# Kernel optimization log

Measured on AMD Instinct MI355X. Metric: run time of the kernel, lower is better.

## Reference

```python
import jax, jax.numpy as jnp
import numpy as np

B, N, D, H = 64, 196, 768, 3072
QMAX = 127.0  # 8-bit symmetric: clamp to [-128, 127]


def ste_round(x):
    # straight-through-estimator round (QAT)
    return x + jax.lax.stop_gradient(jnp.round(x) - x)


def q_linear_diag(x, w, b, a_sf):
    """Quantized diagonal linear (ResMLP Affine / LayerScale as QuantLinear)."""
    w_sf = jnp.max(jnp.abs(w)) / QMAX            # per-tensor weight scale
    w_int = ste_round(w / w_sf)                  # int8 weights (|.|<=127)
    out_int = (x / a_sf) * w_int
    if b is not None:
        out_int = out_int + ste_round(b / (a_sf * w_sf))  # 32-bit bias
    return out_int * (a_sf * w_sf), w_sf


def q_linear_dense(x, w, b, a_sf):
    """Quantized dense linear: int8 GEMM + int32 bias, dequant with a_sf*w_sf."""
    w_sf = jnp.max(jnp.abs(w)) / QMAX
    w_int = jnp.clip(ste_round(w / w_sf), -QMAX - 1, QMAX)
    out_int = jnp.einsum('...i,oi->...o', x / a_sf, w_int) + ste_round(b / (a_sf * w_sf))
    return out_int * (a_sf * w_sf), w_sf


def q_act(x, pre_sf, new_sf, identity=None, id_sf=None):
    """HAWQ-style QuantAct: fixed-point requantization to scale new_sf (8-bit)."""
    if identity is None:
        z_int = ste_round(x / pre_sf)
        out_int = ste_round(z_int * (pre_sf / new_sf))
    else:
        # main branch (x - identity) requantized with pre_sf, identity with id_sf
        z_int = ste_round((x - identity) / pre_sf)
        out_int = ste_round(z_int * (pre_sf / new_sf)) \
                + ste_round(ste_round(identity / id_sf) * (id_sf / new_sf))
    out_int = jnp.clip(out_int, -QMAX - 1, QMAX)
    return out_int * new_sf, new_sf


def _forward(x, norm1_w, norm1_b, attn_w, attn_b, gamma1_w,
             norm2_w, norm2_b, fc1_w, fc1_b, fc2_w, fc2_b, gamma2_w, act_sfs):
    a_sf = act_sfs[0]
    # --- token-mixing half ---
    identity, id_sf = x, a_sf
    x, w_sf = q_linear_diag(x, norm1_w, norm1_b, a_sf)         # norm1 (affine)
    x = jnp.swapaxes(x, 1, 2)                                  # [B, D, N]
    x, a_sf = q_act(x, a_sf * w_sf, act_sfs[1])                # quant_act1
    x, w_sf = q_linear_dense(x, attn_w, attn_b, a_sf)          # attn (cross-patch)
    x = jnp.swapaxes(x, 1, 2)                                  # [B, N, D]
    x, a_sf = q_act(x, a_sf * w_sf, act_sfs[2])                # quant_act2
    x, w_sf = q_linear_diag(x, gamma1_w, None, a_sf)           # gamma_1 (layerscale)
    x = x + identity
    x, a_sf = q_act(x, a_sf * w_sf, act_sfs[3], identity, id_sf)  # quant_act_int32_1
    # --- MLP half ---
    identity, id_sf = x, a_sf
    x, w_sf = q_linear_diag(x, norm2_w, norm2_b, a_sf)         # norm2
    x, a_sf = q_act(x, a_sf * w_sf, act_sfs[4])                # quant_act3
    x, w_sf = q_linear_dense(x, fc1_w, fc1_b, a_sf)            # mlp.fc1
    x = jax.nn.relu(x)
    x, a_sf = q_act(x, a_sf * w_sf, act_sfs[5])                # mlp.quant_act1
    x, w_sf = q_linear_dense(x, fc2_w, fc2_b, a_sf)            # mlp.fc2
    x, a_sf = q_act(x, a_sf * w_sf, act_sfs[6])                # mlp.quant_act2
    x, w_sf = q_linear_diag(x, gamma2_w, None, a_sf)           # gamma_2
    x = x + identity
    x, a_sf = q_act(x, a_sf * w_sf, act_sfs[7], identity, id_sf)  # quant_act_int32_2
    return x, a_sf


def setup_inputs() -> dict:
    key = jax.random.key(0)
    ks = jax.random.split(key, 16)
    act_sfs = jax.random.uniform(ks[14], (8,), jnp.float32, 0.02, 0.06)
    x = jax.random.normal(ks[0], (B, N, D), jnp.float32)
    # input is already quantized at scale act_sfs[0]
    x = jnp.clip(jnp.round(x / act_sfs[0]), -128, 127) * act_sfs[0]
    s = 0.05
    return {
        'x': x,
        'norm1_w': 1.0 + s * jax.random.normal(ks[1], (D,), jnp.float32),
        'norm1_b': s * jax.random.normal(ks[2], (D,), jnp.float32),
        'attn_w': jax.random.normal(ks[3], (N, N), jnp.float32) / np.sqrt(N),
        'attn_b': s * jax.random.normal(ks[4], (N,), jnp.float32),
        'gamma1_w': 0.1 + s * jax.random.normal(ks[5], (D,), jnp.float32),
        'norm2_w': 1.0 + s * jax.random.normal(ks[6], (D,), jnp.float32),
        'norm2_b': s * jax.random.normal(ks[7], (D,), jnp.float32),
        'fc1_w': jax.random.normal(ks[8], (H, D), jnp.float32) / np.sqrt(D),
        'fc1_b': s * jax.random.normal(ks[9], (H,), jnp.float32),
        'fc2_w': jax.random.normal(ks[10], (D, H), jnp.float32) / np.sqrt(H),
        'fc2_b': s * jax.random.normal(ks[11], (D,), jnp.float32),
        'gamma2_w': 0.1 + s * jax.random.normal(ks[12], (D,), jnp.float32),
        'act_sfs': act_sfs,
    }


def reference(x, norm1_w, norm1_b, attn_w, attn_b, gamma1_w,
              norm2_w, norm2_b, fc1_w, fc1_b, fc2_w, fc2_b, gamma2_w, act_sfs):
    return _forward(x, norm1_w, norm1_b, attn_w, attn_b, gamma1_w,
                    norm2_w, norm2_b, fc1_w, fc1_b, fc2_w, fc2_b, gamma2_w, act_sfs)
```

## Files before the change

kernel.cpp:

```cpp
#include <hip/hip_runtime.h>

#define B_ 64
#define N_ 196
#define D_ 768
#define H_ 3072
#define M_ (B_*N_)
#define NP 256

typedef int int4v  __attribute__((ext_vector_type(4)));
typedef int int16v __attribute__((ext_vector_type(16)));
typedef signed char i8;

#define WS_MAX 0
#define WS_W1F 16
#define WS_B1F (16+768)
#define WS_G1F (16+768*2)
#define WS_W2F (16+768*3)
#define WS_B2F (16+768*4)
#define WS_G2F (16+768*5)
#define WS_BA  (16+768*6)
#define WS_BF1 (WS_BA+256)
#define WS_BF2 (WS_BF1+3072)
#define OFF_WA   40960ull
#define OFF_FC1  (OFF_WA+65536ull)
#define OFF_FC2  (OFF_FC1+2359296ull)
#define OFF_X2   (OFF_FC2+2359296ull)
#define OFF_Q3   (OFF_X2+9633792ull)
#define OFF_Q4   (OFF_Q3+9633792ull)
#define OFF_Q1T  OFF_Q4
#define OFF_X8   (OFF_Q4+12582912ull)

__device__ __forceinline__ float clamp8(float v){ return fminf(fmaxf(v,-128.f),127.f); }

__device__ __forceinline__ void async16(const void* g, void* l){
    __builtin_amdgcn_global_load_lds((const __attribute__((address_space(1))) void*)g,
                                     (__attribute__((address_space(3))) void*)l, 16, 0, 0);
}

__global__ void k_init(char* ws, const float* __restrict__ act, float* out_tail){
    int id = blockIdx.x*256 + threadIdx.x;
    if (blockIdx.x == 0){
        float* f = (float*)ws;
        if (threadIdx.x < 8) f[WS_MAX+threadIdx.x] = 0.f;
        if (threadIdx.x == 8) *out_tail = act[7];
    }
    if (id < 4096){ int4v z = {0,0,0,0}; ((int4v*)(ws+OFF_WA))[id] = z; }
}

__global__ void k_maxabs(const float* __restrict__ p0, const float* __restrict__ p1,
                         const float* __restrict__ p2, const float* __restrict__ p3,
                         const float* __restrict__ p4, const float* __restrict__ p5,
                         const float* __restrict__ p6, float* wsmax){
    const float* ps[7] = {p0,p1,p2,p3,p4,p5,p6};
    const int    n4s[7] = {192, 9604, 192, 192, 589824, 589824, 192};
    int tid = blockIdx.y;
    const float4* p = (const float4*)ps[tid]; int n4 = n4s[tid];
    float m = 0.f;
    for (int i = blockIdx.x*blockDim.x + threadIdx.x; i < n4; i += gridDim.x*blockDim.x){
        float4 v = p[i];
        m = fmaxf(m, fmaxf(fmaxf(fabsf(v.x),fabsf(v.y)), fmaxf(fabsf(v.z),fabsf(v.w))));
    }
    #pragma unroll
    for (int off = 32; off; off >>= 1) m = fmaxf(m, __shfl_down(m, off, 64));
    __shared__ float red[4];
    int lane = threadIdx.x & 63, wv = threadIdx.x >> 6;
    if (lane == 0) red[wv] = m;
    __syncthreads();
    if (threadIdx.x == 0){
        float mm = red[0];
        for (int w = 1; w < (int)blockDim.x/64; w++) mm = fmaxf(mm, red[w]);
        atomicMax((unsigned*)&wsmax[tid], __float_as_uint(mm));
    }
}

__device__ __forceinline__ size_t cm_off(int o, int k, int KC){
    return (((size_t)(o>>7)*KC + (k>>6))<<13) + (((k>>4)&3)<<11) + ((o&127)<<4) + (k&15);
}

__global__ void k_qweights(const float* __restrict__ n1w, const float* __restrict__ n1b,
                           const float* __restrict__ aw,  const float* __restrict__ ab,
                           const float* __restrict__ g1w, const float* __restrict__ n2w,
                           const float* __restrict__ n2b, const float* __restrict__ f1w,
                           const float* __restrict__ f1b, const float* __restrict__ f2w,
                           const float* __restrict__ f2b, const float* __restrict__ g2w,
                           const float* __restrict__ act, char* ws){
    float* fws = (float*)ws;
    int*   iws = (int*)ws;
    const float* mx = fws + WS_MAX;
    long i = (long)blockIdx.x*blockDim.x + threadIdx.x;
    const long F4 = 589824;
    if (i < F4){ float sf = mx[4]/127.0f;
        float4 v = ((const float4*)f1w)[i];
        int o = (int)(i/192), kb = (int)(i%192)*4;
        unsigned b0 = (unsigned)(unsigned char)(i8)(int)fminf(fmaxf(rintf(v.x/sf),-128.f),127.f);
        unsigned b1 = (unsigned)(unsigned char)(i8)(int)fminf(fmaxf(rintf(v.y/sf),-128.f),127.f);
        unsigned b2 = (unsigned)(unsigned char)(i8)(int)fminf(fmaxf(rintf(v.z/sf),-128.f),127.f);
        unsigned b3 = (unsigned)(unsigned char)(i8)(int)fminf(fmaxf(rintf(v.w/sf),-128.f),127.f);
        *(unsigned*)(ws + OFF_FC1 + cm_off(o, kb, 12)) = b0 | (b1<<8) | (b2<<16) | (b3<<24);
        return; }
    i -= F4;
    if (i < F4){ float sf = mx[5]/127.0f;
        float4 v = ((const float4*)f2w)[i];
        int o = (int)(i/768), kb = (int)(i%768)*4;
        unsigned b0 = (unsigned)(unsigned char)(i8)(int)fminf(fmaxf(rintf(v.x/sf),-128.f),127.f);
        unsigned b1 = (unsigned)(unsigned char)(i8)(int)fminf(fmaxf(rintf(v.y/sf),-128.f),127.f);
        unsigned b2 = (unsigned)(unsigned char)(i8)(int)fminf(fmaxf(rintf(v.z/sf),-128.f),127.f);
        unsigned b3 = (unsigned)(unsigned char)(i8)(int)fminf(fmaxf(rintf(v.w/sf),-128.f),127.f);
        *(unsigned*)(ws + OFF_FC2 + cm_off(o, kb, 48)) = b0 | (b1<<8) | (b2<<16) | (b3<<24);
        return; }
    i -= F4;
    if (i < 38416){ float sf = mx[1]/127.0f;
        int o = (int)(i/196), k = (int)(i%196);
        ((i8*)(ws+OFF_WA))[cm_off(o, k, 4)] =
            (i8)(int)fminf(fmaxf(rintf(aw[i]/sf),-128.f),127.f); return; }
    i -= 38416;
    if (i < 768){ float sf = mx[0]/127.0f; fws[WS_W1F+i] = rintf(n1w[i]/sf); return; }
    i -= 768;
    if (i < 768){ float sf = mx[0]/127.0f; fws[WS_B1F+i] = rintf(n1b[i]/(act[0]*sf)); return; }
    i -= 768;
    if (i < 768){ float sf = mx[2]/127.0f; fws[WS_G1F+i] = rintf(g1w[i]/sf); return; }
    i -= 768;
    if (i < 768){ float sf = mx[3]/127.0f; fws[WS_W2F+i] = rintf(n2w[i]/sf); return; }
    i -= 768;
    if (i < 768){ float sf = mx[3]/127.0f; fws[WS_B2F+i] = rintf(n2b[i]/(act[3]*sf)); return; }
    i -= 768;
    if (i < 768){ float sf = mx[6]/127.0f; fws[WS_G2F+i] = rintf(g2w[i]/sf); return; }
    i -= 768;
    if (i < 196){ float sf = mx[1]/127.0f; iws[WS_BA+i] = (int)rintf(ab[i]/(act[1]*sf)); return; }
    i -= 196;
    if (i < 3072){ float sf = mx[4]/127.0f; iws[WS_BF1+i] = (int)rintf(f1b[i]/(act[4]*sf)); return; }
    i -= 3072;
    if (i < 768){ float sf = mx[5]/127.0f; iws[WS_BF2+i] = (int)rintf(f2b[i]/(act[5]*sf)); return; }
}

__global__ __launch_bounds__(256) void k_stage1(const float* __restrict__ x,
                                                const char* __restrict__ wsc,
                                                char* __restrict__ ws,
                                                const float* __restrict__ act){
    __shared__ i8 T[64][68];
    const float* fws = (const float*)wsc;
    int b = blockIdx.z, n0 = blockIdx.y*64, d0 = blockIdx.x*64;
    int t = threadIdx.x;
    float a0 = act[0];
    float w1sf = fws[WS_MAX+0]/127.0f;
    float r1 = (a0*w1sf)/act[1];
    int dl = (t & 15) * 4;
    int d  = d0 + dl;
    float4 wv = *(const float4*)(fws + WS_W1F + d);
    float4 bv = *(const float4*)(fws + WS_B1F + d);
    i8* x8 = (i8*)(ws + OFF_X8);
    #pragma unroll
    for (int pass = 0; pass < 4; pass++){
        int nl = (t >> 4) + pass*16;
        int n  = n0 + nl;
        i8 q[4] = {0,0,0,0};
        if (n < 196){
            float4 xv = *(const float4*)(x + ((size_t)b*196 + n)*768 + d);
            float i0 = rintf(xv.x/a0), i1 = rintf(xv.y/a0);
            float i2 = rintf(xv.z/a0), i3 = rintf(xv.w/a0);
            *(char4*)(x8 + ((size_t)b*196 + n)*768 + d) =
                make_char4((i8)(int)i0,(i8)(int)i1,(i8)(int)i2,(i8)(int)i3);
            float o0 = rintf(i0*wv.x + bv.x);
            float o1 = rintf(i1*wv.y + bv.y);
            float o2 = rintf(i2*wv.z + bv.z);
            float o3 = rintf(i3*wv.w + bv.w);
            q[0] = (i8)(int)clamp8(rintf(o0*r1));
            q[1] = (i8)(int)clamp8(rintf(o1*r1));
            q[2] = (i8)(int)clamp8(rintf(o2*r1));
            q[3] = (i8)(int)clamp8(rintf(o3*r1));
        }
        T[dl+0][nl] = q[0]; T[dl+1][nl] = q[1];
        T[dl+2][nl] = q[2]; T[dl+3][nl] = q[3];
    }
    __syncthreads();
    i8* q1T = (i8*)(ws + OFF_Q1T) + (size_t)b*196608;
    #pragma unroll
    for (int e = 0; e < 4; e++){
        int id = t + e*256;
        int row = id >> 4, c = (id & 15) * 4;
        int dd = d0 + row;
        int v = *(const int*)&T[row][c];
        size_t dst = (((size_t)(dd>>7)*4 + blockIdx.y)<<13) + ((size_t)(c>>4)<<11)
                     + ((dd&127)<<4) + (c&15);
        *(int*)(q1T + dst) = v;
    }
}

__device__ __forceinline__ void gemm_cm_256(const i8* __restrict__ gA, const i8* __restrict__ gB,
                                            int iters, int4v acc[4][4], i8* As, i8* Bs, int t){
    int lane = t & 63;
    int wm = (t>>6)&1, wn = t>>7;
    int lo = t*16;
    async16(gA + lo,        As + lo);
    async16(gA + 4096 + lo, As + 4096 + lo);
    async16(gB + lo,        Bs + lo);
    async16(gB + 4096 + lo, Bs + 4096 + lo);
    int arow = (lane>>4)*2048 + (wm*64 + (lane&15))*16;
    int brow = (lane>>4)*2048 + (wn*64 + (lane&15))*16;
    for (int i = 0; i < iters; i++){
        __syncthreads();
        if (i+1 < iters){
            int nb = ((i+1)&1) << 13;
            size_t kb = (size_t)(i+1) << 13;
            async16(gA + kb + lo,        As + nb + lo);
            async16(gA + kb + 4096 + lo, As + nb + 4096 + lo);
            async16(gB + kb + lo,        Bs + nb + lo);
            async16(gB + kb + 4096 + lo, Bs + nb + 4096 + lo);
        }
        int cb = (i&1) << 13;
        int4v a[4], bb[4];
        #pragma unroll
        for (int mt = 0; mt < 4; mt++)
            a[mt] = *(const int4v*)(As + cb + arow + mt*256);
        #pragma unroll
        for (int nt = 0; nt < 4; nt++)
            bb[nt] = *(const int4v*)(Bs + cb + brow + nt*256);
        #pragma unroll
        for (int mt = 0; mt < 4; mt++)
            #pragma unroll
            for (int nt = 0; nt < 4; nt++)
                acc[mt][nt] = __builtin_amdgcn_mfma_i32_16x16x64_i8(a[mt], bb[nt], acc[mt][nt], 0,0,0);
    }
}

__device__ __forceinline__ void gemm32_cm_pipe(const i8* __restrict__ gA, const i8* __restrict__ gB,
                                               int iters, int16v acc[2][2], i8* lds, int t){
    int lane = t & 63;
    int wm = (t>>6)&1, wn = t>>7;
    int lo = t*16;
    auto stage = [&](int s, int buf){
        size_t kb = (size_t)s << 13;
        i8* L = lds + buf*16384;
        async16(gA + kb + lo,        L + lo);
        async16(gA + kb + 4096 + lo, L + 4096 + lo);
        async16(gB + kb + lo,        L + 8192 + lo);
        async16(gB + kb + 4096 + lo, L + 12288 + lo);
    };
    stage(0, 0);
    if (iters > 1) stage(1, 1);
    int arow = (lane>>5)*2048 + (wm*64 + (lane&31))*16;
    int brow = 8192 + (lane>>5)*2048 + (wn*64 + (lane&31))*16;
    int buf = 0;
    for (int i = 0; i < iters; i++){
        if (i+1 < iters) asm volatile("s_waitcnt vmcnt(4)" ::: "memory");
        else             asm volatile("s_waitcnt vmcnt(0)" ::: "memory");
        __builtin_amdgcn_s_barrier();
        __builtin_amdgcn_sched_barrier(0);
        if (i+2 < iters){
            int b2 = buf + 2; if (b2 >= 3) b2 -= 3;
            stage(i+2, b2);
        }
        const i8* L = lds + buf*16384;
        int4v a[2][2], bb[2][2];
        #pragma unroll
        for (int kk = 0; kk < 2; kk++){
            #pragma unroll
            for (int mt = 0; mt < 2; mt++){
                a[kk][mt]  = *(const int4v*)(L + kk*4096 + arow + mt*512);
                bb[kk][mt] = *(const int4v*)(L + kk*4096 + brow + mt*512);
            }
        }
        #pragma unroll
        for (int mt = 0; mt < 2; mt++)
            #pragma unroll
            for (int nt = 0; nt < 2; nt++)
                #pragma unroll
                for (int kk = 0; kk < 2; kk++)
                    acc[mt][nt] = __builtin_amdgcn_mfma_i32_32x32x32_i8(a[kk][mt], bb[kk][nt], acc[mt][nt], 0,0,0);
        buf++; if (buf == 3) buf = 0;
    }
}

__global__ __launch_bounds__(256) void k_attn(const char* __restrict__ ws,
                                              const float* __restrict__ act){
    __shared__ char smem[32768];
    const float* fws = (const float*)ws;
    const int*   iws = (const int*)ws;
    int b = blockIdx.z;
    int m0 = blockIdx.x*128, n0 = blockIdx.y*128;
    const i8* gA = (const i8*)(ws + OFF_WA)  + ((size_t)(m0>>7))*32768;
    const i8* gB = (const i8*)(ws + OFF_Q1T) + (size_t)b*196608 + ((size_t)(n0>>7))*32768;
    const i8* x8 = (const i8*)(ws + OFF_X8);
    i8* x2  = (i8*)(ws + OFF_X2);
    i8* q3  = (i8*)(ws + OFF_Q3);
    int t = threadIdx.x, lane = t & 63;
    int wm = (t>>6)&1, wn = t>>7;
    int4v acc[4][4]; int4v zz = {0,0,0,0};
    #pragma unroll
    for (int mt=0;mt<4;mt++) for (int nt=0;nt<4;nt++) acc[mt][nt] = zz;
    gemm_cm_256(gA, gB, 4, acc, (i8*)smem, (i8*)smem+16384, t);

    float a1=act[1], a2=act[2], a3=act[3], a4=act[4];
    float wasf = fws[WS_MAX+1]/127.0f; float r2  = (a1*wasf)/a2;
    float g1sf = fws[WS_MAX+2]/127.0f; float r3a = (a2*g1sf)/a3; float r3b = act[0]/a3;
    float w2sf = fws[WS_MAX+3]/127.0f; float r4  = (a3*w2sf)/a4;
    float g1v[4], w2v[4], b2v[4];
    #pragma unroll
    for (int nt=0;nt<4;nt++){
        int d = n0 + wn*64 + nt*16 + (lane&15);
        g1v[nt] = fws[WS_G1F + d]; w2v[nt] = fws[WS_W2F + d]; b2v[nt] = fws[WS_B2F + d];
    }
    __syncthreads();
    i8* Xs = (i8*)smem;
    i8* Qs = (i8*)smem + 16384;
    #pragma unroll
    for (int mt=0;mt<4;mt++){
        #pragma unroll
        for (int r=0;r<4;r++){
            int ml = wm*64 + mt*16 + (lane>>4)*4 + r;
            int o  = m0 + ml;
            int ba = iws[WS_BA + o];
            #pragma unroll
            for (int nt=0;nt<4;nt++){
                int nl = wn*64 + nt*16 + (lane&15);
                int d  = n0 + nl;
                float s2 = (float)(acc[mt][nt][r] + ba);
                float q2 = clamp8(rintf(s2*r2));
                float o3v = q2*g1v[nt];
                float idi = (o < 196) ? (float)x8[((size_t)b*196 + o)*768 + d] : 0.f;
                float tt = rintf(o3v*r3a) + rintf(idi*r3b);
                tt = clamp8(tt);
                float o4 = tt*w2v[nt] + b2v[nt];
                float qr = clamp8(rintf(o4*r4));
                Xs[ml*128 + nl] = (i8)(int)tt;
                Qs[ml*128 + nl] = (i8)(int)qr;
            }
        }
    }
    __syncthreads();
    #pragma unroll
    for (int e=0;e<4;e++){
        int id = t + e*256;
        int row = id>>3, c = id&7;
        int o = m0 + row;
        if (o < 196){
            int rg = b*196 + o;
            size_t g = (size_t)rg*768 + n0 + c*16;
            *(int4v*)(x2 + g) = *(const int4v*)(Xs + row*128 + c*16);
            size_t dst = (((size_t)(rg>>7)*12 + (n0>>6) + (c>>2))<<13)
                         + ((size_t)(c&3)<<11) + ((rg&127)<<4);
            *(int4v*)(q3 + dst) = *(const int4v*)(Qs + row*128 + c*16);
        }
    }
}

__global__ __launch_bounds__(256,3) void k_fc1(const char* __restrict__ ws, const float* __restrict__ act){
    __shared__ char smem[49152];
    const float* fws = (const float*)ws;
    const int*   iws = (const int*)ws;
    int n0 = blockIdx.y*128;
    const i8* gA = (const i8*)(ws+OFF_Q3)  + ((size_t)blockIdx.x)*12*8192;
    const i8* gB = (const i8*)(ws+OFF_FC1) + ((size_t)blockIdx.y)*12*8192;
    const int* bias = iws + WS_BF1;
    i8* q4 = (i8*)(ws+OFF_Q4);
    int t = threadIdx.x, lane = t & 63;
    int wm = (t>>6)&1, wn = t>>7;
    int16v acc[2][2];
    int16v zz = {0,0,0,0,0,0,0,0,0,0,0,0,0,0,0,0};
    #pragma unroll
    for (int mt=0;mt<2;mt++) for (int nt=0;nt<2;nt++) acc[mt][nt] = zz;
    gemm32_cm_pipe(gA, gB, 12, acc, (i8*)smem, t);
    float wsf = fws[WS_MAX+4]/127.0f;
    float r5 = (act[4]*wsf)/act[5];
    int bcol[2];
    #pragma unroll
    for (int nt=0;nt<2;nt++) bcol[nt] = bias[n0 + wn*64 + nt*32 + (lane&31)];
    i8* Cs = (i8*)smem;
    #pragma unroll
    for (int mt=0;mt<2;mt++){
        #pragma unroll
        for (int nt=0;nt<2;nt++){
            int nl = wn*64 + nt*32 + (lane&31);
            #pragma unroll
            for (int r=0;r<16;r++){
                int s = acc[mt][nt][r] + bcol[nt];
                if (s < 0) s = 0;
                float q = clamp8(rintf((float)s * r5));
                int ml = wm*64 + mt*32 + 4*(lane>>5) + (r&3) + 8*(r>>2);
                Cs[ml*128 + nl] = (i8)(int)q;
            }
        }
    }
    __syncthreads();
    #pragma unroll
    for (int e=0;e<4;e++){
        int id = t + e*256;
        int row = id>>3, c = id&7;
        size_t dst = (((size_t)blockIdx.x*48 + (n0>>6) + (c>>2))<<13)
                     + ((size_t)(c&3)<<11) + ((size_t)row<<4);
        *(int4v*)(q4 + dst) = *(const int4v*)(Cs + row*128 + c*16);
    }
}

__global__ __launch_bounds__(256,3) void k_fc2(const char* __restrict__ ws, const float* __restrict__ act,
                                               float* __restrict__ out){
    __shared__ char smem[49152];
    const float* fws = (const float*)ws;
    const int*   iws = (const int*)ws;
    int m0 = blockIdx.x*128, n0 = blockIdx.y*128;
    const i8* gA = (const i8*)(ws+OFF_Q4)  + ((size_t)blockIdx.x)*48*8192;
    const i8* gB = (const i8*)(ws+OFF_FC2) + ((size_t)blockIdx.y)*48*8192;
    const int* bias = iws + WS_BF2;
    const float* g2f = fws + WS_G2F;
    const i8* x2 = (const i8*)(ws+OFF_X2);
    int t = threadIdx.x, lane = t & 63;
    int wm = (t>>6)&1, wn = t>>7;
    int16v acc[2][2];
    int16v zz = {0,0,0,0,0,0,0,0,0,0,0,0,0,0,0,0};
    #pragma unroll
    for (int mt=0;mt<2;mt++) for (int nt=0;nt<2;nt++) acc[mt][nt] = zz;
    gemm32_cm_pipe(gA, gB, 48, acc, (i8*)smem, t);
    float a3=act[3], a5=act[5], a6=act[6], a7=act[7];
    float wsf  = fws[WS_MAX+5]/127.0f; float r6  = (a5*wsf)/a6;
    float g2sf = fws[WS_MAX+6]/127.0f; float r7a = (a6*g2sf)/a7; float r7b = a3/a7;
    int bcol[2]; float g2v[2];
    #pragma unroll
    for (int nt=0;nt<2;nt++){
        int nc = n0 + wn*64 + nt*32 + (lane&31);
        bcol[nt] = bias[nc]; g2v[nt] = g2f[nc];
    }
    #pragma unroll
    for (int mt=0;mt<2;mt++){
        #pragma unroll
        for (int nt=0;nt<2;nt++){
            int nc = n0 + wn*64 + nt*32 + (lane&31);
            #pragma unroll
            for (int r=0;r<16;r++){
                int ml = wm*64 + mt*32 + 4*(lane>>5) + (r&3) + 8*(r>>2);
                size_t gi = (size_t)(m0+ml)*768 + nc;
                int s = acc[mt][nt][r] + bcol[nt];
                float q6 = clamp8(rintf((float)s*r6));
                float o7 = q6*g2v[nt];
                float idi = (float)x2[gi];
                float tt = rintf(o7*r7a) + rintf(idi*r7b);
                tt = clamp8(tt);
                out[gi] = tt*a7;
            }
        }
    }
}

extern "C" void kernel_launch(void* const* d_in, const int* in_sizes, int n_in,
                              void* d_out, int out_size, void* d_ws, size_t ws_size,
                              hipStream_t stream){
    const float* x   = (const float*)d_in[0];
    const float* n1w = (const float*)d_in[1];
    const float* n1b = (const float*)d_in[2];
    const float* aw  = (const float*)d_in[3];
    const float* ab  = (const float*)d_in[4];
    const float* g1w = (const float*)d_in[5];
    const float* n2w = (const float*)d_in[6];
    const float* n2b = (const float*)d_in[7];
    const float* f1w = (const float*)d_in[8];
    const float* f1b = (const float*)d_in[9];
    const float* f2w = (const float*)d_in[10];
    const float* f2b = (const float*)d_in[11];
    const float* g2w = (const float*)d_in[12];
    const float* act = (const float*)d_in[13];
    char* ws = (char*)d_ws;
    float* out = (float*)d_out;

    k_init<<<16,256,0,stream>>>(ws, act, out + (size_t)B_*N_*D_);
    k_maxabs<<<dim3(120,7),256,0,stream>>>(n1w, aw, g1w, n2w, f1w, f2w, g2w, (float*)ws);
    long qwThreads = 2L*589824 + 38416 + 768L*6 + 196 + 3072 + 768;
    k_qweights<<<(int)((qwThreads+255)/256),256,0,stream>>>(n1w,n1b,aw,ab,g1w,n2w,n2b,
                                                            f1w,f1b,f2w,f2b,g2w,act,ws);
    k_stage1<<<dim3(12,4,64),256,0,stream>>>(x, ws, ws, act);
    k_attn<<<dim3(2,6,64),256,0,stream>>>(ws, act);
    k_fc1<<<dim3(98,24),256,0,stream>>>(ws, act);
    k_fc2<<<dim3(98,6),256,0,stream>>>(ws, act, out);
}
```

Baseline: 259.1 us.

## Switch fc1/fc2 GEMM to BK=128 double-buffered pipeline

```diff
diff --git a/kernel.cpp b/kernel.cpp
--- a/kernel.cpp
+++ b/kernel.cpp
@@ -223,51 +223,43 @@
     }
 }
 
-__device__ __forceinline__ void gemm32_cm_pipe(const i8* __restrict__ gA, const i8* __restrict__ gB,
-                                               int iters, int16v acc[2][2], i8* lds, int t){
+__device__ __forceinline__ void gemm32_cm_bk128(const i8* __restrict__ gA, const i8* __restrict__ gB,
+                                                int iters, int16v acc[2][2], i8* lds, int t){
     int lane = t & 63;
     int wm = (t>>6)&1, wn = t>>7;
     int lo = t*16;
     auto stage = [&](int s, int buf){
-        size_t kb = (size_t)s << 13;
-        i8* L = lds + buf*16384;
-        async16(gA + kb + lo,        L + lo);
-        async16(gA + kb + 4096 + lo, L + 4096 + lo);
-        async16(gB + kb + lo,        L + 8192 + lo);
-        async16(gB + kb + 4096 + lo, L + 12288 + lo);
+        size_t kb = (size_t)s << 14;
+        i8* L = lds + buf*32768;
+        #pragma unroll
+        for (int j = 0; j < 4; j++){
+            async16(gA + kb + j*4096 + lo, L + j*4096 + lo);
+            async16(gB + kb + j*4096 + lo, L + 16384 + j*4096 + lo);
+        }
     };
     stage(0, 0);
-    if (iters > 1) stage(1, 1);
     int arow = (lane>>5)*2048 + (wm*64 + (lane&31))*16;
-    int brow = 8192 + (lane>>5)*2048 + (wn*64 + (lane&31))*16;
-    int buf = 0;
+    int brow = 16384 + (lane>>5)*2048 + (wn*64 + (lane&31))*16;
     for (int i = 0; i < iters; i++){
-        if (i+1 < iters) asm volatile("s_waitcnt vmcnt(4)" ::: "memory");
-        else             asm volatile("s_waitcnt vmcnt(0)" ::: "memory");
+        asm volatile("s_waitcnt vmcnt(0)" ::: "memory");
         __builtin_amdgcn_s_barrier();
         __builtin_amdgcn_sched_barrier(0);
-        if (i+2 < iters){
-            int b2 = buf + 2; if (b2 >= 3) b2 -= 3;
-            stage(i+2, b2);
-        }
-        const i8* L = lds + buf*16384;
-        int4v a[2][2], bb[2][2];
-        #pragma unroll
-        for (int kk = 0; kk < 2; kk++){
+        if (i+1 < iters) stage(i+1, (i+1)&1);
+        const i8* L = lds + (i&1)*32768;
+        #pragma unroll
+        for (int kk = 0; kk < 4; kk++){
+            int4v a[2], bb[2];
             #pragma unroll
             for (int mt = 0; mt < 2; mt++){
-                a[kk][mt]  = *(const int4v*)(L + kk*4096 + arow + mt*512);
-                bb[kk][mt] = *(const int4v*)(L + kk*4096 + brow + mt*512);
+                a[mt]  = *(const int4v*)(L + kk*4096 + arow + mt*512);
+                bb[mt] = *(const int4v*)(L + kk*4096 + brow + mt*512);
             }
-        }
-        #pragma unroll
-        for (int mt = 0; mt < 2; mt++)
-            #pragma unroll
-            for (int nt = 0; nt < 2; nt++)
+            #pragma unroll
+            for (int mt = 0; mt < 2; mt++)
                 #pragma unroll
-                for (int kk = 0; kk < 2; kk++)
-                    acc[mt][nt] = __builtin_amdgcn_mfma_i32_32x32x32_i8(a[kk][mt], bb[kk][nt], acc[mt][nt], 0,0,0);
-        buf++; if (buf == 3) buf = 0;
+                for (int nt = 0; nt < 2; nt++)
+                    acc[mt][nt] = __builtin_amdgcn_mfma_i32_32x32x32_i8(a[mt], bb[nt], acc[mt][nt], 0,0,0);
+        }
     }
 }
 
@@ -344,8 +336,8 @@
     }
 }
 
-__global__ __launch_bounds__(256,3) void k_fc1(const char* __restrict__ ws, const float* __restrict__ act){
-    __shared__ char smem[49152];
+__global__ __launch_bounds__(256,2) void k_fc1(const char* __restrict__ ws, const float* __restrict__ act){
+    __shared__ char smem[65536];
     const float* fws = (const float*)ws;
     const int*   iws = (const int*)ws;
     int n0 = blockIdx.y*128;
@@ -359,7 +351,7 @@
     int16v zz = {0,0,0,0,0,0,0,0,0,0,0,0,0,0,0,0};
     #pragma unroll
     for (int mt=0;mt<2;mt++) for (int nt=0;nt<2;nt++) acc[mt][nt] = zz;
-    gemm32_cm_pipe(gA, gB, 12, acc, (i8*)smem, t);
+    gemm32_cm_bk128(gA, gB, 6, acc, (i8*)smem, t);
     float wsf = fws[WS_MAX+4]/127.0f;
     float r5 = (act[4]*wsf)/act[5];
     int bcol[2];
@@ -392,9 +384,9 @@
     }
 }
 
-__global__ __launch_bounds__(256,3) void k_fc2(const char* __restrict__ ws, const float* __restrict__ act,
+__global__ __launch_bounds__(256,2) void k_fc2(const char* __restrict__ ws, const float* __restrict__ act,
                                                float* __restrict__ out){
-    __shared__ char smem[49152];
+    __shared__ char smem[65536];
     const float* fws = (const float*)ws;
     const int*   iws = (const int*)ws;
     int m0 = blockIdx.x*128, n0 = blockIdx.y*128;
@@ -409,7 +401,7 @@
     int16v zz = {0,0,0,0,0,0,0,0,0,0,0,0,0,0,0,0};
     #pragma unroll
     for (int mt=0;mt<2;mt++) for (int nt=0;nt<2;nt++) acc[mt][nt] = zz;
-    gemm32_cm_pipe(gA, gB, 48, acc, (i8*)smem, t);
+    gemm32_cm_bk128(gA, gB, 24, acc, (i8*)smem, t);
     float a3=act[3], a5=act[5], a6=act[6], a7=act[7];
     float wsf  = fws[WS_MAX+5]/127.0f; float r6  = (a5*wsf)/a6;
     float g2sf = fws[WS_MAX+6]/127.0f; float r7a = (a6*g2sf)/a7; float r7b = a3/a7;
```

Result: slower. 271.3 us (+4.7%).

## Remap GEMM workgroups across XCDs for L2 locality and replace init kernel with memsets

Applied to the files above, without the earlier changes.

```diff
diff --git a/kernel.cpp b/kernel.cpp
--- a/kernel.cpp
+++ b/kernel.cpp
@@ -37,20 +37,12 @@
                                      (__attribute__((address_space(3))) void*)l, 16, 0, 0);
 }
 
-__global__ void k_init(char* ws, const float* __restrict__ act, float* out_tail){
-    int id = blockIdx.x*256 + threadIdx.x;
-    if (blockIdx.x == 0){
-        float* f = (float*)ws;
-        if (threadIdx.x < 8) f[WS_MAX+threadIdx.x] = 0.f;
-        if (threadIdx.x == 8) *out_tail = act[7];
-    }
-    if (id < 4096){ int4v z = {0,0,0,0}; ((int4v*)(ws+OFF_WA))[id] = z; }
-}
-
 __global__ void k_maxabs(const float* __restrict__ p0, const float* __restrict__ p1,
                          const float* __restrict__ p2, const float* __restrict__ p3,
                          const float* __restrict__ p4, const float* __restrict__ p5,
-                         const float* __restrict__ p6, float* wsmax){
+                         const float* __restrict__ p6, float* wsmax,
+                         const float* __restrict__ act, float* out_tail){
+    if (blockIdx.x == 0 && blockIdx.y == 0 && threadIdx.x == 0) *out_tail = act[7];
     const float* ps[7] = {p0,p1,p2,p3,p4,p5,p6};
     const int    n4s[7] = {192, 9604, 192, 192, 589824, 589824, 192};
     int tid = blockIdx.y;
@@ -276,8 +268,11 @@
     __shared__ char smem[32768];
     const float* fws = (const float*)ws;
     const int*   iws = (const int*)ws;
-    int b = blockIdx.z;
-    int m0 = blockIdx.x*128, n0 = blockIdx.y*128;
+    int orig = blockIdx.x;
+    int wg = (orig & 7) * 96 + (orig >> 3);
+    int b  = wg / 12;
+    int r  = wg % 12;
+    int m0 = (r & 1) * 128, n0 = (r >> 1) * 128;
     const i8* gA = (const i8*)(ws + OFF_WA)  + ((size_t)(m0>>7))*32768;
     const i8* gB = (const i8*)(ws + OFF_Q1T) + (size_t)b*196608 + ((size_t)(n0>>7))*32768;
     const i8* x8 = (const i8*)(ws + OFF_X8);
@@ -306,15 +301,15 @@
     #pragma unroll
     for (int mt=0;mt<4;mt++){
         #pragma unroll
-        for (int r=0;r<4;r++){
-            int ml = wm*64 + mt*16 + (lane>>4)*4 + r;
+        for (int r4i=0;r4i<4;r4i++){
+            int ml = wm*64 + mt*16 + (lane>>4)*4 + r4i;
             int o  = m0 + ml;
             int ba = iws[WS_BA + o];
             #pragma unroll
             for (int nt=0;nt<4;nt++){
                 int nl = wn*64 + nt*16 + (lane&15);
                 int d  = n0 + nl;
-                float s2 = (float)(acc[mt][nt][r] + ba);
+                float s2 = (float)(acc[mt][nt][r4i] + ba);
                 float q2 = clamp8(rintf(s2*r2));
                 float o3v = q2*g1v[nt];
                 float idi = (o < 196) ? (float)x8[((size_t)b*196 + o)*768 + d] : 0.f;
@@ -348,9 +343,13 @@
     __shared__ char smem[49152];
     const float* fws = (const float*)ws;
     const int*   iws = (const int*)ws;
-    int n0 = blockIdx.y*128;
-    const i8* gA = (const i8*)(ws+OFF_Q3)  + ((size_t)blockIdx.x)*12*8192;
-    const i8* gB = (const i8*)(ws+OFF_FC1) + ((size_t)blockIdx.y)*12*8192;
+    int orig = blockIdx.x;
+    int wg = (orig & 7) * 294 + (orig >> 3);
+    int bx = wg / 24;
+    int by = wg % 24;
+    int n0 = by*128;
+    const i8* gA = (const i8*)(ws+OFF_Q3)  + ((size_t)bx)*12*8192;
+    const i8* gB = (const i8*)(ws+OFF_FC1) + ((size_t)by)*12*8192;
     const int* bias = iws + WS_BF1;
     i8* q4 = (i8*)(ws+OFF_Q4);
     int t = threadIdx.x, lane = t & 63;
@@ -386,7 +385,7 @@
     for (int e=0;e<4;e++){
         int id = t + e*256;
         int row = id>>3, c = id&7;
-        size_t dst = (((size_t)blockIdx.x*48 + (n0>>6) + (c>>2))<<13)
+        size_t dst = (((size_t)bx*48 + (n0>>6) + (c>>2))<<13)
                      + ((size_t)(c&3)<<11) + ((size_t)row<<4);
         *(int4v*)(q4 + dst) = *(const int4v*)(Cs + row*128 + c*16);
     }
@@ -397,9 +396,14 @@
     __shared__ char smem[49152];
     const float* fws = (const float*)ws;
     const int*   iws = (const int*)ws;
-    int m0 = blockIdx.x*128, n0 = blockIdx.y*128;
-    const i8* gA = (const i8*)(ws+OFF_Q4)  + ((size_t)blockIdx.x)*48*8192;
-    const i8* gB = (const i8*)(ws+OFF_FC2) + ((size_t)blockIdx.y)*48*8192;
+    int orig = blockIdx.x;
+    int xcd = orig & 7, lid = orig >> 3;
+    int wg = (xcd < 4 ? xcd*74 : 296 + (xcd-4)*73) + lid;
+    int bx = wg / 6;
+    int by = wg % 6;
+    int m0 = bx*128, n0 = by*128;
+    const i8* gA = (const i8*)(ws+OFF_Q4)  + ((size_t)bx)*48*8192;
+    const i8* gB = (const i8*)(ws+OFF_FC2) + ((size_t)by)*48*8192;
     const int* bias = iws + WS_BF2;
     const float* g2f = fws + WS_G2F;
     const i8* x2 = (const i8*)(ws+OFF_X2);
@@ -460,13 +464,15 @@
     char* ws = (char*)d_ws;
     float* out = (float*)d_out;
 
-    k_init<<<16,256,0,stream>>>(ws, act, out + (size_t)B_*N_*D_);
-    k_maxabs<<<dim3(120,7),256,0,stream>>>(n1w, aw, g1w, n2w, f1w, f2w, g2w, (float*)ws);
+    hipMemsetAsync(ws, 0, 32, stream);
+    hipMemsetAsync(ws + OFF_WA, 0, 65536, stream);
+    k_maxabs<<<dim3(120,7),256,0,stream>>>(n1w, aw, g1w, n2w, f1w, f2w, g2w, (float*)ws,
+                                           act, out + (size_t)B_*N_*D_);
     long qwThreads = 2L*589824 + 38416 + 768L*6 + 196 + 3072 + 768;
     k_qweights<<<(int)((qwThreads+255)/256),256,0,stream>>>(n1w,n1b,aw,ab,g1w,n2w,n2b,
                                                             f1w,f1b,f2w,f2b,g2w,act,ws);
     k_stage1<<<dim3(12,4,64),256,0,stream>>>(x, ws, ws, act);
-    k_attn<<<dim3(2,6,64),256,0,stream>>>(ws, act);
-    k_fc1<<<dim3(98,24),256,0,stream>>>(ws, act);
-    k_fc2<<<dim3(98,6),256,0,stream>>>(ws, act, out);
-}
+    k_attn<<<768,256,0,stream>>>(ws, act);
+    k_fc1<<<2352,256,0,stream>>>(ws, act);
+    k_fc2<<<588,256,0,stream>>>(ws, act, out);
+}
```

After: 268.1 us. 1.03x slower.

## Enlarge fc1 tile to 256x128 and remap workgroups per XCD for fc1/fc2

Applied to the files above, without the earlier changes.

```diff
diff --git a/kernel.cpp b/kernel.cpp
--- a/kernel.cpp
+++ b/kernel.cpp
@@ -344,30 +344,70 @@
     }
 }
 
-__global__ __launch_bounds__(256,3) void k_fc1(const char* __restrict__ ws, const float* __restrict__ act){
+__global__ __launch_bounds__(256,2) void k_fc1(const char* __restrict__ ws, const float* __restrict__ act){
     __shared__ char smem[49152];
     const float* fws = (const float*)ws;
     const int*   iws = (const int*)ws;
-    int n0 = blockIdx.y*128;
-    const i8* gA = (const i8*)(ws+OFF_Q3)  + ((size_t)blockIdx.x)*12*8192;
-    const i8* gB = (const i8*)(ws+OFF_FC1) + ((size_t)blockIdx.y)*12*8192;
+    int orig = blockIdx.x;
+    int wg = (orig & 7) * 147 + (orig >> 3);
+    int bx = wg / 24;
+    int by = wg % 24;
+    int n0 = by*128;
+    const i8* gA = (const i8*)(ws+OFF_Q3)  + (size_t)bx*2*98304;
+    const i8* gB = (const i8*)(ws+OFF_FC1) + (size_t)by*98304;
     const int* bias = iws + WS_BF1;
     i8* q4 = (i8*)(ws+OFF_Q4);
     int t = threadIdx.x, lane = t & 63;
     int wm = (t>>6)&1, wn = t>>7;
-    int16v acc[2][2];
+    int lo = t*16;
+    int16v acc[4][2];
     int16v zz = {0,0,0,0,0,0,0,0,0,0,0,0,0,0,0,0};
     #pragma unroll
-    for (int mt=0;mt<2;mt++) for (int nt=0;nt<2;nt++) acc[mt][nt] = zz;
-    gemm32_cm_pipe(gA, gB, 12, acc, (i8*)smem, t);
+    for (int mt=0;mt<4;mt++) for (int nt=0;nt<2;nt++) acc[mt][nt] = zz;
+    auto stage = [&](int s, int buf){
+        size_t kb = (size_t)s << 13;
+        i8* L = (i8*)smem + buf*24576;
+        async16(gA + kb + lo,                 L + lo);
+        async16(gA + kb + 4096 + lo,          L + 4096 + lo);
+        async16(gA + 98304 + kb + lo,         L + 8192 + lo);
+        async16(gA + 98304 + kb + 4096 + lo,  L + 12288 + lo);
+        async16(gB + kb + lo,                 L + 16384 + lo);
+        async16(gB + kb + 4096 + lo,          L + 20480 + lo);
+    };
+    stage(0, 0);
+    int arow = wm*8192  + (lane>>5)*2048 + (lane&31)*16;
+    int brow = 16384 + (lane>>5)*2048 + (wn*64 + (lane&31))*16;
+    for (int i = 0; i < 12; i++){
+        asm volatile("s_waitcnt vmcnt(0)" ::: "memory");
+        __builtin_amdgcn_s_barrier();
+        __builtin_amdgcn_sched_barrier(0);
+        if (i+1 < 12) stage(i+1, (i+1)&1);
+        const i8* L = (const i8*)smem + (i&1)*24576;
+        #pragma unroll
+        for (int kk = 0; kk < 2; kk++){
+            int4v a[4], bb[2];
+            #pragma unroll
+            for (int mt = 0; mt < 4; mt++)
+                a[mt] = *(const int4v*)(L + kk*4096 + arow + mt*512);
+            #pragma unroll
+            for (int nt = 0; nt < 2; nt++)
+                bb[nt] = *(const int4v*)(L + kk*4096 + brow + nt*512);
+            #pragma unroll
+            for (int mt = 0; mt < 4; mt++)
+                #pragma unroll
+                for (int nt = 0; nt < 2; nt++)
+                    acc[mt][nt] = __builtin_amdgcn_mfma_i32_32x32x32_i8(a[mt], bb[nt], acc[mt][nt], 0,0,0);
+        }
+    }
     float wsf = fws[WS_MAX+4]/127.0f;
     float r5 = (act[4]*wsf)/act[5];
     int bcol[2];
     #pragma unroll
     for (int nt=0;nt<2;nt++) bcol[nt] = bias[n0 + wn*64 + nt*32 + (lane&31)];
+    __syncthreads();
     i8* Cs = (i8*)smem;
     #pragma unroll
-    for (int mt=0;mt<2;mt++){
+    for (int mt=0;mt<4;mt++){
         #pragma unroll
         for (int nt=0;nt<2;nt++){
             int nl = wn*64 + nt*32 + (lane&31);
@@ -376,18 +416,18 @@
                 int s = acc[mt][nt][r] + bcol[nt];
                 if (s < 0) s = 0;
                 float q = clamp8(rintf((float)s * r5));
-                int ml = wm*64 + mt*32 + 4*(lane>>5) + (r&3) + 8*(r>>2);
+                int ml = wm*128 + mt*32 + 4*(lane>>5) + (r&3) + 8*(r>>2);
                 Cs[ml*128 + nl] = (i8)(int)q;
             }
         }
     }
     __syncthreads();
     #pragma unroll
-    for (int e=0;e<4;e++){
+    for (int e=0;e<8;e++){
         int id = t + e*256;
         int row = id>>3, c = id&7;
-        size_t dst = (((size_t)blockIdx.x*48 + (n0>>6) + (c>>2))<<13)
-                     + ((size_t)(c&3)<<11) + ((size_t)row<<4);
+        size_t dst = (((size_t)(bx*2 + (row>>7))*48 + (n0>>6) + (c>>2))<<13)
+                     + ((size_t)(c&3)<<11) + ((size_t)(row&127)<<4);
         *(int4v*)(q4 + dst) = *(const int4v*)(Cs + row*128 + c*16);
     }
 }
@@ -397,9 +437,14 @@
     __shared__ char smem[49152];
     const float* fws = (const float*)ws;
     const int*   iws = (const int*)ws;
-    int m0 = blockIdx.x*128, n0 = blockIdx.y*128;
-    const i8* gA = (const i8*)(ws+OFF_Q4)  + ((size_t)blockIdx.x)*48*8192;
-    const i8* gB = (const i8*)(ws+OFF_FC2) + ((size_t)blockIdx.y)*48*8192;
+    int orig = blockIdx.x;
+    int xcd = orig & 7, lid = orig >> 3;
+    int wg = (xcd < 4 ? xcd*74 : 296 + (xcd-4)*73) + lid;
+    int bx = wg / 6;
+    int by = wg % 6;
+    int m0 = bx*128, n0 = by*128;
+    const i8* gA = (const i8*)(ws+OFF_Q4)  + ((size_t)bx)*48*8192;
+    const i8* gB = (const i8*)(ws+OFF_FC2) + ((size_t)by)*48*8192;
     const int* bias = iws + WS_BF2;
     const float* g2f = fws + WS_G2F;
     const i8* x2 = (const i8*)(ws+OFF_X2);
@@ -467,6 +512,6 @@
                                                             f1w,f1b,f2w,f2b,g2w,act,ws);
     k_stage1<<<dim3(12,4,64),256,0,stream>>>(x, ws, ws, act);
     k_attn<<<dim3(2,6,64),256,0,stream>>>(ws, act);
-    k_fc1<<<dim3(98,24),256,0,stream>>>(ws, act);
-    k_fc2<<<dim3(98,6),256,0,stream>>>(ws, act, out);
-}
+    k_fc1<<<1176,256,0,stream>>>(ws, act);
+    k_fc2<<<588,256,0,stream>>>(ws, act, out);
+}
```

Result: no change. 257.7 us (-0.6%).
